# Kernel tuning notes

Measured on AMD Instinct MI355X. Metric: run time of the kernel, lower is better.

The kernel has to match this reference:

```python
import jax, jax.numpy as jnp
import numpy as np

EPS = 1e-5
N_NODES = 50000


def sage_conv(x, src, dst, Wl, Wr, b):
    # mean-aggregate source features at destination nodes, then two linears
    msgs = x[src]  # [E, F] irregular gather
    agg = jax.ops.segment_sum(msgs, dst, num_segments=N_NODES)
    cnt = jax.ops.segment_sum(jnp.ones((src.shape[0], 1), x.dtype), dst,
                              num_segments=N_NODES)
    agg = agg / jnp.maximum(cnt, 1.0)
    return agg @ Wl + x @ Wr + b


def batch_norm(h, gamma, beta):
    mu = jnp.mean(h, axis=0)
    var = jnp.mean((h - mu) ** 2, axis=0)  # biased var, as torch BN training
    return (h - mu) * jax.lax.rsqrt(var + EPS) * gamma + beta


def setup_inputs() -> dict:
    key = jax.random.key(0)
    ks = jax.random.split(key, 16)
    d_in, d_h, n_cls, n_edges = 128, 128, 2, 600000
    s = lambda fan: 1.0 / np.sqrt(fan)
    inp = {
        "x": jax.random.normal(ks[0], (N_NODES, d_in), jnp.float32),
        "edge_index": jax.random.randint(ks[1], (2, n_edges), 0, N_NODES, jnp.int64),
        "W_l0": jax.random.uniform(ks[2], (d_in, d_h), jnp.float32, -s(d_in), s(d_in)),
        "W_r0": jax.random.uniform(ks[3], (d_in, d_h), jnp.float32, -s(d_in), s(d_in)),
        "b0": jnp.zeros((d_h,), jnp.float32),
        "g0": jnp.ones((d_h,), jnp.float32),
        "be0": jnp.zeros((d_h,), jnp.float32),
        "W_l1": jax.random.uniform(ks[4], (d_h, d_h), jnp.float32, -s(d_h), s(d_h)),
        "W_r1": jax.random.uniform(ks[5], (d_h, d_h), jnp.float32, -s(d_h), s(d_h)),
        "b1": jnp.zeros((d_h,), jnp.float32),
        "g1": jnp.ones((d_h,), jnp.float32),
        "be1": jnp.zeros((d_h,), jnp.float32),
        "W_out": jax.random.uniform(ks[6], (d_h, n_cls), jnp.float32, -s(d_h), s(d_h)),
        "b_out": jnp.zeros((n_cls,), jnp.float32),
    }
    return inp


def reference(x, edge_index, W_l0, W_r0, b0, g0, be0,
              W_l1, W_r1, b1, g1, be1, W_out, b_out):
    src, dst = edge_index[0], edge_index[1]
    # layer 0: SAGEConv -> BN -> ReLU (dropout = identity in eval/reference)
    h = sage_conv(x, src, dst, W_l0, W_r0, b0)
    h = jax.nn.relu(batch_norm(h, g0, be0))
    # layer 1
    h = sage_conv(h, src, dst, W_l1, W_r1, b1)
    h = jax.nn.relu(batch_norm(h, g1, be1))
    return h @ W_out + b_out
```

## Files before the change

### kernel.cpp

```cpp
#include <hip/hip_runtime.h>
#include <hip/hip_bf16.h>

#define F 128

typedef __attribute__((ext_vector_type(8))) short short8;
typedef __attribute__((ext_vector_type(4))) float floatx4;

__device__ __forceinline__ float bf_lo(unsigned u) { return __uint_as_float(u << 16); }
__device__ __forceinline__ float bf_hi(unsigned u) { return __uint_as_float(u & 0xffff0000u); }

__device__ __forceinline__ unsigned short f2bf(float x) {
  unsigned u = __float_as_uint(x);
  u += 0x7fffu + ((u >> 16) & 1u);
  return (unsigned short)(u >> 16);
}
__device__ __forceinline__ unsigned pack2(float a, float b) {
  return (unsigned)f2bf(a) | ((unsigned)f2bf(b) << 16);
}

__global__ __launch_bounds__(256) void k_count(const int* __restrict__ dst,
                                               int* __restrict__ A, int E) {
  int e = blockIdx.x * 256 + threadIdx.x;
  if (e < E) atomicAdd(&A[dst[e]], 1);
}

__global__ __launch_bounds__(1024) void k_scanA(int* __restrict__ A,
                                                int* __restrict__ bsum, int n) {
  __shared__ int wtot[16];
  int t = threadIdx.x, l = t & 63, w = t >> 6;
  int i = blockIdx.x * 1024 + t;
  int v = (i < n) ? A[i] : 0;
  int acc = v;
#pragma unroll
  for (int off = 1; off < 64; off <<= 1) {
    int u = __shfl_up(acc, off);
    if (l >= off) acc += u;
  }
  if (l == 63) wtot[w] = acc;
  __syncthreads();
  int woff = 0, total = 0;
#pragma unroll
  for (int ww = 0; ww < 16; ++ww) {
    total += wtot[ww];
    if (ww < w) woff += wtot[ww];
  }
  if (i < n) A[i] = woff + (acc - v);
  if (t == 0) bsum[blockIdx.x] = total;
}

__global__ __launch_bounds__(1024) void k_scanC(int* __restrict__ A,
                                                const int* __restrict__ bsum, int n, int nb) {
  __shared__ int sbase;
  int t = threadIdx.x;
  if (t < 64) {
    int v = (t < nb) ? bsum[t] : 0;
    int acc = v;
#pragma unroll
    for (int off = 1; off < 64; off <<= 1) {
      int u = __shfl_up(acc, off);
      if (t >= off) acc += u;
    }
    int base = (blockIdx.x == 0) ? 0 : __shfl(acc, blockIdx.x - 1);
    if (t == 0) sbase = base;
  }
  __syncthreads();
  int i = blockIdx.x * 1024 + t;
  if (i < n) A[i] += sbase;
}

__global__ __launch_bounds__(256) void k_fill(const int* __restrict__ srcT,
                                              const int* __restrict__ dst,
                                              int* __restrict__ A, int* __restrict__ adj, int E) {
  int e = blockIdx.x * 256 + threadIdx.x;
  if (e >= E) return;
  int s = srcT[e], d = dst[e];
  int slot = atomicAdd(&A[d], 1);
  adj[slot] = s;
}

__global__ __launch_bounds__(256) void k_prep(const float* __restrict__ x,
                                              const float* __restrict__ Wl0,
                                              const float* __restrict__ Wr0,
                                              const float* __restrict__ Wl1,
                                              const float* __restrict__ Wr1,
                                              unsigned short* __restrict__ xb,
                                              unsigned short* __restrict__ WcatT0,
                                              unsigned short* __restrict__ WcatT1, int n4) {
  int i = blockIdx.x * 256 + threadIdx.x;
  if (i < n4) {
    float4 v = ((const float4*)x)[i];
    ((ushort4*)xb)[i] = make_ushort4(f2bf(v.x), f2bf(v.y), f2bf(v.z), f2bf(v.w));
  } else {
    int j = i - n4;
    if (j < 2 * 256 * F) {
      int layer = j >> 15;
      int jj = j & 32767;
      int k = jj >> 7, n = jj & (F - 1);
      const float* Wl = layer ? Wl1 : Wl0;
      const float* Wr = layer ? Wr1 : Wr0;
      unsigned short* WT = layer ? WcatT1 : WcatT0;
      float v = (k < F) ? Wl[k * F + n] : Wr[(k - F) * F + n];
      WT[(size_t)n * 256 + k] = f2bf(v);
    }
  }
}

__global__ __launch_bounds__(256) void k_gather(const unsigned short* __restrict__ xin,
                                                const int* __restrict__ A,
                                                const int* __restrict__ adj,
                                                unsigned short* __restrict__ aggb, int N) {
  int d = blockIdx.x * 4 + (threadIdx.x >> 6);
  if (d >= N) return;
  int l = threadIdx.x & 63;
  int grp = l >> 4, ln = l & 15;
  int e0 = (d == 0) ? 0 : A[d - 1];
  int e1 = A[d];
  int deg = e1 - e0;
  const uint4* xrows = (const uint4*)xin;
  float acc[8] = {0.f, 0.f, 0.f, 0.f, 0.f, 0.f, 0.f, 0.f};
  if (deg > 0) {
    int ids = adj[min(e0 + l, e1 - 1)];
    int m = min(deg, 64);
    for (int j0 = 0; j0 < m; j0 += 4) {
      int jj = j0 + grp;
      int s = __shfl(ids, jj);
      if (jj < m) {
        uint4 u = xrows[(size_t)s * 16 + ln];
        acc[0] += bf_lo(u.x); acc[1] += bf_hi(u.x);
        acc[2] += bf_lo(u.y); acc[3] += bf_hi(u.y);
        acc[4] += bf_lo(u.z); acc[5] += bf_hi(u.z);
        acc[6] += bf_lo(u.w); acc[7] += bf_hi(u.w);
      }
    }
    for (int e = e0 + 64 + grp; e < e1; e += 4) {
      int s = adj[e];
      uint4 u = xrows[(size_t)s * 16 + ln];
      acc[0] += bf_lo(u.x); acc[1] += bf_hi(u.x);
      acc[2] += bf_lo(u.y); acc[3] += bf_hi(u.y);
      acc[4] += bf_lo(u.z); acc[5] += bf_hi(u.z);
      acc[6] += bf_lo(u.w); acc[7] += bf_hi(u.w);
    }
  }
#pragma unroll
  for (int k2 = 0; k2 < 8; ++k2) {
    acc[k2] += __shfl_xor(acc[k2], 16);
    acc[k2] += __shfl_xor(acc[k2], 32);
  }
  if (grp == 0) {
    float inv = 1.0f / fmaxf((float)deg, 1.0f);
    uint4 o = make_uint4(pack2(acc[0] * inv, acc[1] * inv), pack2(acc[2] * inv, acc[3] * inv),
                         pack2(acc[4] * inv, acc[5] * inv), pack2(acc[6] * inv, acc[7] * inv));
    ((uint4*)aggb)[(size_t)d * 16 + ln] = o;
  }
}

__global__ __launch_bounds__(256, 2) void k_gemm(
    const unsigned short* __restrict__ aggb, const unsigned short* __restrict__ xb,
    const unsigned short* __restrict__ WcatT, const float* __restrict__ bias,
    unsigned short* __restrict__ hb, float* __restrict__ pbuf, int N) {
  const int w = threadIdx.x >> 6;
  const int l = threadIdx.x & 63;
  const int lm = l & 15;
  const int lq = l >> 4;
  const int cbase = 32 * w;

  short8 bfrag[2][8];
#pragma unroll
  for (int c = 0; c < 2; ++c) {
    int col = cbase + 16 * c + lm;
    const unsigned short* wp = WcatT + (size_t)col * 256 + lq * 8;
#pragma unroll
    for (int s = 0; s < 8; ++s) bfrag[c][s] = *(const short8*)(wp + 32 * s);
  }
  float bcol0 = bias[cbase + lm];
  float bcol1 = bias[cbase + 16 + lm];
  float bsum0 = 0.f, bsum1 = 0.f, bsq0 = 0.f, bsq1 = 0.f;

  int r0 = blockIdx.x * 64;
  floatx4 acc[4][2] = {};
#pragma unroll
  for (int t = 0; t < 4; ++t) {
    int r = r0 + 16 * t + lm;
    const unsigned short* arow = aggb + (size_t)r * F + lq * 8;
    const unsigned short* xrow = xb + (size_t)r * F + lq * 8;
    short8 af[8];
#pragma unroll
    for (int s = 0; s < 4; ++s) {
      af[s] = *(const short8*)(arow + 32 * s);
      af[s + 4] = *(const short8*)(xrow + 32 * s);
    }
#pragma unroll
    for (int s = 0; s < 8; ++s) {
      acc[t][0] = __builtin_amdgcn_mfma_f32_16x16x32_bf16(af[s], bfrag[0][s], acc[t][0], 0, 0, 0);
      acc[t][1] = __builtin_amdgcn_mfma_f32_16x16x32_bf16(af[s], bfrag[1][s], acc[t][1], 0, 0, 0);
    }
  }
#pragma unroll
  for (int t = 0; t < 4; ++t) {
#pragma unroll
    for (int c = 0; c < 2; ++c) {
      int col = cbase + 16 * c + lm;
      float bc = c ? bcol1 : bcol0;
#pragma unroll
      for (int g = 0; g < 4; ++g) {
        int row = r0 + 16 * t + lq * 4 + g;
        if (row < N) {
          float v = acc[t][c][g] + bc;
          hb[(size_t)row * F + col] = f2bf(v);
          if (c) { bsum1 += v; bsq1 += v * v; }
          else   { bsum0 += v; bsq0 += v * v; }
        }
      }
    }
  }
  bsum0 += __shfl_xor(bsum0, 16); bsum0 += __shfl_xor(bsum0, 32);
  bsq0  += __shfl_xor(bsq0, 16);  bsq0  += __shfl_xor(bsq0, 32);
  bsum1 += __shfl_xor(bsum1, 16); bsum1 += __shfl_xor(bsum1, 32);
  bsq1  += __shfl_xor(bsq1, 16);  bsq1  += __shfl_xor(bsq1, 32);
  if (lq == 0) {
    float* pb = pbuf + (size_t)blockIdx.x * 256;
    pb[cbase + lm]            = bsum0;
    pb[128 + cbase + lm]      = bsq0;
    pb[cbase + 16 + lm]       = bsum1;
    pb[128 + cbase + 16 + lm] = bsq1;
  }
}

__global__ __launch_bounds__(256) void k_bnstats(const float* __restrict__ pbuf,
                                                 const float* __restrict__ g,
                                                 const float* __restrict__ be,
                                                 float* __restrict__ stats,
                                                 float* __restrict__ scale,
                                                 float* __restrict__ shift,
                                                 float invN, int nb) {
  int t = threadIdx.x;
  float s = 0.f;
  for (int b = blockIdx.x; b < nb; b += 8) s += pbuf[(size_t)b * 256 + t];
  atomicAdd(&stats[t], s);
  __threadfence();
  __syncthreads();
  __shared__ int lastS;
  if (t == 0) {
    int ticket = atomicAdd((int*)(stats + 256), 1);
    lastS = (ticket == 7);
  }
  __syncthreads();
  if (lastS) {
    __threadfence();
    if (t < 128) {
      float sum = __hip_atomic_load(&stats[t], __ATOMIC_RELAXED, __HIP_MEMORY_SCOPE_AGENT);
      float sq  = __hip_atomic_load(&stats[t + 128], __ATOMIC_RELAXED, __HIP_MEMORY_SCOPE_AGENT);
      float mu = sum * invN;
      float var = fmaxf(sq * invN - mu * mu, 0.0f);
      float sc = g[t] * rsqrtf(var + 1e-5f);
      scale[t] = sc;
      shift[t] = be[t] - mu * sc;
    }
  }
}

__global__ __launch_bounds__(256) void k_bnrelu(const unsigned short* __restrict__ h,
                                                unsigned short* __restrict__ dst,
                                                const float* __restrict__ scale,
                                                const float* __restrict__ shift, int n8) {
  int i = blockIdx.x * 256 + threadIdx.x;
  if (i >= n8) return;
  uint4 u = ((const uint4*)h)[i];
  int g = i & 15;
  float4 sc0 = ((const float4*)scale)[2 * g];
  float4 sc1 = ((const float4*)scale)[2 * g + 1];
  float4 sh0 = ((const float4*)shift)[2 * g];
  float4 sh1 = ((const float4*)shift)[2 * g + 1];
  unsigned o0 = pack2(fmaxf(fmaf(bf_lo(u.x), sc0.x, sh0.x), 0.f),
                      fmaxf(fmaf(bf_hi(u.x), sc0.y, sh0.y), 0.f));
  unsigned o1 = pack2(fmaxf(fmaf(bf_lo(u.y), sc0.z, sh0.z), 0.f),
                      fmaxf(fmaf(bf_hi(u.y), sc0.w, sh0.w), 0.f));
  unsigned o2 = pack2(fmaxf(fmaf(bf_lo(u.z), sc1.x, sh1.x), 0.f),
                      fmaxf(fmaf(bf_hi(u.z), sc1.y, sh1.y), 0.f));
  unsigned o3 = pack2(fmaxf(fmaf(bf_lo(u.w), sc1.z, sh1.z), 0.f),
                      fmaxf(fmaf(bf_hi(u.w), sc1.w, sh1.w), 0.f));
  ((uint4*)dst)[i] = make_uint4(o0, o1, o2, o3);
}

__global__ __launch_bounds__(256) void k_bnout(const unsigned short* __restrict__ hb,
                                               const float* __restrict__ scale,
                                               const float* __restrict__ shift,
                                               const float* __restrict__ Wout,
                                               const float* __restrict__ bout,
                                               float* __restrict__ out, int N) {
  __shared__ float W0s[F], W1s[F];
  int t = threadIdx.x;
  if (t < F) {
    W0s[t] = Wout[2 * t];
    W1s[t] = Wout[2 * t + 1];
  }
  __syncthreads();
  int r = blockIdx.x * 16 + (t >> 4);
  int ln = t & 15;
  if (r >= N) return;
  uint4 u = ((const uint4*)(hb + (size_t)r * F))[ln];
  float4 sc0 = ((const float4*)scale)[2 * ln];
  float4 sc1 = ((const float4*)scale)[2 * ln + 1];
  float4 sh0 = ((const float4*)shift)[2 * ln];
  float4 sh1 = ((const float4*)shift)[2 * ln + 1];
  float v[8];
  v[0] = fmaxf(fmaf(bf_lo(u.x), sc0.x, sh0.x), 0.f);
  v[1] = fmaxf(fmaf(bf_hi(u.x), sc0.y, sh0.y), 0.f);
  v[2] = fmaxf(fmaf(bf_lo(u.y), sc0.z, sh0.z), 0.f);
  v[3] = fmaxf(fmaf(bf_hi(u.y), sc0.w, sh0.w), 0.f);
  v[4] = fmaxf(fmaf(bf_lo(u.z), sc1.x, sh1.x), 0.f);
  v[5] = fmaxf(fmaf(bf_hi(u.z), sc1.y, sh1.y), 0.f);
  v[6] = fmaxf(fmaf(bf_lo(u.w), sc1.z, sh1.z), 0.f);
  v[7] = fmaxf(fmaf(bf_hi(u.w), sc1.w, sh1.w), 0.f);
  float a0 = 0.f, a1 = 0.f;
#pragma unroll
  for (int j = 0; j < 8; ++j) {
    a0 += v[j] * W0s[8 * ln + j];
    a1 += v[j] * W1s[8 * ln + j];
  }
#pragma unroll
  for (int off = 1; off < 16; off <<= 1) {
    a0 += __shfl_xor(a0, off);
    a1 += __shfl_xor(a1, off);
  }
  if (ln == 0) {
    out[2 * r]     = a0 + bout[0];
    out[2 * r + 1] = a1 + bout[1];
  }
}

extern "C" void kernel_launch(void* const* d_in, const int* in_sizes, int n_in,
                              void* d_out, int out_size, void* d_ws, size_t ws_size,
                              hipStream_t stream) {
  const float* x   = (const float*)d_in[0];
  const int*   eix = (const int*)d_in[1];
  const float* Wl0 = (const float*)d_in[2];
  const float* Wr0 = (const float*)d_in[3];
  const float* b0  = (const float*)d_in[4];
  const float* g0  = (const float*)d_in[5];
  const float* be0 = (const float*)d_in[6];
  const float* Wl1 = (const float*)d_in[7];
  const float* Wr1 = (const float*)d_in[8];
  const float* b1  = (const float*)d_in[9];
  const float* g1  = (const float*)d_in[10];
  const float* be1 = (const float*)d_in[11];
  const float* Wo  = (const float*)d_in[12];
  const float* bo  = (const float*)d_in[13];

  int N = in_sizes[0] / F;
  int E = in_sizes[1] / 2;
  const int* src  = eix;
  const int* dstv = eix + E;

  int nRowBlocks = (N + 63) / 64;
  size_t Npad = (size_t)nRowBlocks * 64;
  int nScanB = (N + 1023) / 1024;

  unsigned short* aggb   = (unsigned short*)d_ws;
  unsigned short* xb     = aggb + Npad * F;
  unsigned short* hb     = xb + Npad * F;
  unsigned short* WcatT0 = hb + Npad * F;
  unsigned short* WcatT1 = WcatT0 + 256 * F;
  float* scale  = (float*)(WcatT1 + 256 * F);
  float* shift  = scale + F;
  int*   A      = (int*)(shift + F);
  int*   bsum   = A + N;
  float* stats0 = (float*)(bsum + 64);
  float* stats1 = stats0 + 257;
  int*   adj    = (int*)(stats1 + 257);
  float* pbuf   = (float*)(adj + E);

  hipMemsetAsync(A, 0, (size_t)(N + 64 + 514) * sizeof(int), stream);

  k_count<<<(E + 255) / 256, 256, 0, stream>>>(dstv, A, E);
  k_scanA<<<nScanB, 1024, 0, stream>>>(A, bsum, N);
  k_scanC<<<nScanB, 1024, 0, stream>>>(A, bsum, N, nScanB);
  k_fill<<<(E + 255) / 256, 256, 0, stream>>>(src, dstv, A, adj, E);

  int n4 = N * F / 4, n8 = N * F / 8;
  k_prep<<<(n4 + 2 * 256 * F + 255) / 256, 256, 0, stream>>>(x, Wl0, Wr0, Wl1, Wr1,
                                                             xb, WcatT0, WcatT1, n4);

  k_gather<<<(N + 3) / 4, 256, 0, stream>>>(xb, A, adj, aggb, N);
  k_gemm<<<nRowBlocks, 256, 0, stream>>>(aggb, xb, WcatT0, b0, hb, pbuf, N);
  k_bnstats<<<8, 256, 0, stream>>>(pbuf, g0, be0, stats0, scale, shift, 1.0f / N, nRowBlocks);
  k_bnrelu<<<(n8 + 255) / 256, 256, 0, stream>>>(hb, xb, scale, shift, n8);

  k_gather<<<(N + 3) / 4, 256, 0, stream>>>(xb, A, adj, aggb, N);
  k_gemm<<<nRowBlocks, 256, 0, stream>>>(aggb, xb, WcatT1, b1, hb, pbuf, N);
  k_bnstats<<<8, 256, 0, stream>>>(pbuf, g1, be1, stats1, scale, shift, 1.0f / N, nRowBlocks);

  k_bnout<<<(N + 15) / 16, 256, 0, stream>>>(hb, scale, shift, Wo, bo, (float*)d_out, N);
}
```

Baseline: 343.2 us.

## Fuse neighbor gather, GEMM and BN stats into one per-layer kernel

Each layer's mean-aggregation gather now writes its bf16 result into LDS, and the same block runs the MFMA GEMM from there. The separate global agg buffer and its write/read round-trip go away. BN statistics reduction moves into the layer kernel's tail via a last-block ticket, and the degree-count kernel is merged into the prep conversion kernel, cutting launches. The risk is that the gather phase, now inside a 2-occupancy GEMM kernel holding register-resident weight fragments, may get less latency hiding. The last block also serially sums all per-block partials.

```diff
diff --git a/kernel.cpp b/kernel.cpp
--- a/kernel.cpp
+++ b/kernel.cpp
@@ -18,75 +18,22 @@
   return (unsigned)f2bf(a) | ((unsigned)f2bf(b) << 16);
 }
 
-__global__ __launch_bounds__(256) void k_count(const int* __restrict__ dst,
-                                               int* __restrict__ A, int E) {
-  int e = blockIdx.x * 256 + threadIdx.x;
-  if (e < E) atomicAdd(&A[dst[e]], 1);
-}
-
-__global__ __launch_bounds__(1024) void k_scanA(int* __restrict__ A,
-                                                int* __restrict__ bsum, int n) {
-  __shared__ int wtot[16];
-  int t = threadIdx.x, l = t & 63, w = t >> 6;
-  int i = blockIdx.x * 1024 + t;
-  int v = (i < n) ? A[i] : 0;
-  int acc = v;
-#pragma unroll
-  for (int off = 1; off < 64; off <<= 1) {
-    int u = __shfl_up(acc, off);
-    if (l >= off) acc += u;
-  }
-  if (l == 63) wtot[w] = acc;
-  __syncthreads();
-  int woff = 0, total = 0;
-#pragma unroll
-  for (int ww = 0; ww < 16; ++ww) {
-    total += wtot[ww];
-    if (ww < w) woff += wtot[ww];
-  }
-  if (i < n) A[i] = woff + (acc - v);
-  if (t == 0) bsum[blockIdx.x] = total;
-}
-
-__global__ __launch_bounds__(1024) void k_scanC(int* __restrict__ A,
-                                                const int* __restrict__ bsum, int n, int nb) {
-  __shared__ int sbase;
-  int t = threadIdx.x;
-  if (t < 64) {
-    int v = (t < nb) ? bsum[t] : 0;
-    int acc = v;
-#pragma unroll
-    for (int off = 1; off < 64; off <<= 1) {
-      int u = __shfl_up(acc, off);
-      if (t >= off) acc += u;
-    }
-    int base = (blockIdx.x == 0) ? 0 : __shfl(acc, blockIdx.x - 1);
-    if (t == 0) sbase = base;
-  }
-  __syncthreads();
-  int i = blockIdx.x * 1024 + t;
-  if (i < n) A[i] += sbase;
-}
-
-__global__ __launch_bounds__(256) void k_fill(const int* __restrict__ srcT,
-                                              const int* __restrict__ dst,
-                                              int* __restrict__ A, int* __restrict__ adj, int E) {
-  int e = blockIdx.x * 256 + threadIdx.x;
-  if (e >= E) return;
-  int s = srcT[e], d = dst[e];
-  int slot = atomicAdd(&A[d], 1);
-  adj[slot] = s;
-}
-
-__global__ __launch_bounds__(256) void k_prep(const float* __restrict__ x,
-                                              const float* __restrict__ Wl0,
-                                              const float* __restrict__ Wr0,
-                                              const float* __restrict__ Wl1,
-                                              const float* __restrict__ Wr1,
-                                              unsigned short* __restrict__ xb,
-                                              unsigned short* __restrict__ WcatT0,
-                                              unsigned short* __restrict__ WcatT1, int n4) {
-  int i = blockIdx.x * 256 + threadIdx.x;
+__global__ __launch_bounds__(256) void k_pre(const int* __restrict__ dst, int* __restrict__ A,
+                                             int E, int cb,
+                                             const float* __restrict__ x,
+                                             const float* __restrict__ Wl0,
+                                             const float* __restrict__ Wr0,
+                                             const float* __restrict__ Wl1,
+                                             const float* __restrict__ Wr1,
+                                             unsigned short* __restrict__ xb,
+                                             unsigned short* __restrict__ WcatT0,
+                                             unsigned short* __restrict__ WcatT1, int n4) {
+  if (blockIdx.x < cb) {
+    int e = blockIdx.x * 256 + threadIdx.x;
+    if (e < E) atomicAdd(&A[dst[e]], 1);
+    return;
+  }
+  int i = (blockIdx.x - cb) * 256 + threadIdx.x;
   if (i < n4) {
     float4 v = ((const float4*)x)[i];
     ((ushort4*)xb)[i] = make_ushort4(f2bf(v.x), f2bf(v.y), f2bf(v.z), f2bf(v.w));
@@ -105,84 +52,143 @@
   }
 }
 
-__global__ __launch_bounds__(256) void k_gather(const unsigned short* __restrict__ xin,
-                                                const int* __restrict__ A,
-                                                const int* __restrict__ adj,
-                                                unsigned short* __restrict__ aggb, int N) {
-  int d = blockIdx.x * 4 + (threadIdx.x >> 6);
-  if (d >= N) return;
-  int l = threadIdx.x & 63;
-  int grp = l >> 4, ln = l & 15;
-  int e0 = (d == 0) ? 0 : A[d - 1];
-  int e1 = A[d];
-  int deg = e1 - e0;
-  const uint4* xrows = (const uint4*)xin;
-  float acc[8] = {0.f, 0.f, 0.f, 0.f, 0.f, 0.f, 0.f, 0.f};
-  if (deg > 0) {
-    int ids = adj[min(e0 + l, e1 - 1)];
-    int m = min(deg, 64);
-    for (int j0 = 0; j0 < m; j0 += 4) {
-      int jj = j0 + grp;
-      int s = __shfl(ids, jj);
-      if (jj < m) {
-        uint4 u = xrows[(size_t)s * 16 + ln];
-        acc[0] += bf_lo(u.x); acc[1] += bf_hi(u.x);
-        acc[2] += bf_lo(u.y); acc[3] += bf_hi(u.y);
-        acc[4] += bf_lo(u.z); acc[5] += bf_hi(u.z);
-        acc[6] += bf_lo(u.w); acc[7] += bf_hi(u.w);
+__global__ __launch_bounds__(1024) void k_scanA(int* __restrict__ A,
+                                                int* __restrict__ bsum, int n) {
+  __shared__ int wtot[16];
+  int t = threadIdx.x, l = t & 63, w = t >> 6;
+  int i = blockIdx.x * 1024 + t;
+  int v = (i < n) ? A[i] : 0;
+  int acc = v;
+#pragma unroll
+  for (int off = 1; off < 64; off <<= 1) {
+    int u = __shfl_up(acc, off);
+    if (l >= off) acc += u;
+  }
+  if (l == 63) wtot[w] = acc;
+  __syncthreads();
+  int woff = 0, total = 0;
+#pragma unroll
+  for (int ww = 0; ww < 16; ++ww) {
+    total += wtot[ww];
+    if (ww < w) woff += wtot[ww];
+  }
+  if (i < n) A[i] = woff + (acc - v);
+  if (t == 0) bsum[blockIdx.x] = total;
+}
+
+__global__ __launch_bounds__(1024) void k_scanC(int* __restrict__ A,
+                                                const int* __restrict__ bsum, int n, int nb) {
+  __shared__ int sbase;
+  int t = threadIdx.x;
+  if (t < 64) {
+    int v = (t < nb) ? bsum[t] : 0;
+    int acc = v;
+#pragma unroll
+    for (int off = 1; off < 64; off <<= 1) {
+      int u = __shfl_up(acc, off);
+      if (t >= off) acc += u;
+    }
+    int base = (blockIdx.x == 0) ? 0 : __shfl(acc, blockIdx.x - 1);
+    if (t == 0) sbase = base;
+  }
+  __syncthreads();
+  int i = blockIdx.x * 1024 + t;
+  if (i < n) A[i] += sbase;
+}
+
+__global__ __launch_bounds__(256) void k_fill(const int* __restrict__ srcT,
+                                              const int* __restrict__ dst,
+                                              int* __restrict__ A, int* __restrict__ adj, int E) {
+  int e = blockIdx.x * 256 + threadIdx.x;
+  if (e >= E) return;
+  int s = srcT[e], d = dst[e];
+  int slot = atomicAdd(&A[d], 1);
+  adj[slot] = s;
+}
+
+__global__ __launch_bounds__(256, 2) void k_layer(
+    const unsigned short* __restrict__ xin, const int* __restrict__ A,
+    const int* __restrict__ adj, const unsigned short* __restrict__ WcatT,
+    const float* __restrict__ bias, unsigned short* __restrict__ hb,
+    float* __restrict__ pbuf, int* __restrict__ ticket,
+    const float* __restrict__ g, const float* __restrict__ be,
+    float* __restrict__ scale, float* __restrict__ shift,
+    float invN, int N, int nb) {
+  __shared__ unsigned short aggS[64][136];
+  __shared__ float red[256];
+  __shared__ int lastS;
+  const int tid = threadIdx.x;
+  const int w = tid >> 6, l = tid & 63;
+  const int grp = l >> 4, ln = l & 15;
+  const int cbase = 32 * w;
+  const int r0 = blockIdx.x * 64;
+
+  short8 bfrag[2][8];
+#pragma unroll
+  for (int c = 0; c < 2; ++c) {
+    int col = cbase + 16 * c + ln;
+    const unsigned short* wp = WcatT + (size_t)col * 256 + grp * 8;
+#pragma unroll
+    for (int s = 0; s < 8; ++s) bfrag[c][s] = *(const short8*)(wp + 32 * s);
+  }
+  float bcol0 = bias[cbase + ln];
+  float bcol1 = bias[cbase + 16 + ln];
+
+  const uint4* xrows4 = (const uint4*)xin;
+#pragma unroll 1
+  for (int i = 0; i < 16; ++i) {
+    int dd = w + 4 * i;
+    int d = r0 + dd;
+    float acc[8] = {0.f, 0.f, 0.f, 0.f, 0.f, 0.f, 0.f, 0.f};
+    int deg = 0;
+    if (d < N) {
+      int e0 = (d == 0) ? 0 : A[d - 1];
+      int e1 = A[d];
+      deg = e1 - e0;
+      if (deg > 0) {
+        int ids = adj[min(e0 + l, e1 - 1)];
+        int m = min(deg, 64);
+        for (int j0 = 0; j0 < m; j0 += 4) {
+          int jj = j0 + grp;
+          int s = __shfl(ids, jj);
+          if (jj < m) {
+            uint4 u = xrows4[(size_t)s * 16 + ln];
+            acc[0] += bf_lo(u.x); acc[1] += bf_hi(u.x);
+            acc[2] += bf_lo(u.y); acc[3] += bf_hi(u.y);
+            acc[4] += bf_lo(u.z); acc[5] += bf_hi(u.z);
+            acc[6] += bf_lo(u.w); acc[7] += bf_hi(u.w);
+          }
+        }
+        for (int e = e0 + 64 + grp; e < e1; e += 4) {
+          int s = adj[e];
+          uint4 u = xrows4[(size_t)s * 16 + ln];
+          acc[0] += bf_lo(u.x); acc[1] += bf_hi(u.x);
+          acc[2] += bf_lo(u.y); acc[3] += bf_hi(u.y);
+          acc[4] += bf_lo(u.z); acc[5] += bf_hi(u.z);
+          acc[6] += bf_lo(u.w); acc[7] += bf_hi(u.w);
+        }
       }
     }
-    for (int e = e0 + 64 + grp; e < e1; e += 4) {
-      int s = adj[e];
-      uint4 u = xrows[(size_t)s * 16 + ln];
-      acc[0] += bf_lo(u.x); acc[1] += bf_hi(u.x);
-      acc[2] += bf_lo(u.y); acc[3] += bf_hi(u.y);
-      acc[4] += bf_lo(u.z); acc[5] += bf_hi(u.z);
-      acc[6] += bf_lo(u.w); acc[7] += bf_hi(u.w);
-    }
-  }
-#pragma unroll
-  for (int k2 = 0; k2 < 8; ++k2) {
-    acc[k2] += __shfl_xor(acc[k2], 16);
-    acc[k2] += __shfl_xor(acc[k2], 32);
-  }
-  if (grp == 0) {
-    float inv = 1.0f / fmaxf((float)deg, 1.0f);
-    uint4 o = make_uint4(pack2(acc[0] * inv, acc[1] * inv), pack2(acc[2] * inv, acc[3] * inv),
-                         pack2(acc[4] * inv, acc[5] * inv), pack2(acc[6] * inv, acc[7] * inv));
-    ((uint4*)aggb)[(size_t)d * 16 + ln] = o;
-  }
-}
-
-__global__ __launch_bounds__(256, 2) void k_gemm(
-    const unsigned short* __restrict__ aggb, const unsigned short* __restrict__ xb,
-    const unsigned short* __restrict__ WcatT, const float* __restrict__ bias,
-    unsigned short* __restrict__ hb, float* __restrict__ pbuf, int N) {
-  const int w = threadIdx.x >> 6;
-  const int l = threadIdx.x & 63;
-  const int lm = l & 15;
-  const int lq = l >> 4;
-  const int cbase = 32 * w;
-
-  short8 bfrag[2][8];
-#pragma unroll
-  for (int c = 0; c < 2; ++c) {
-    int col = cbase + 16 * c + lm;
-    const unsigned short* wp = WcatT + (size_t)col * 256 + lq * 8;
-#pragma unroll
-    for (int s = 0; s < 8; ++s) bfrag[c][s] = *(const short8*)(wp + 32 * s);
-  }
-  float bcol0 = bias[cbase + lm];
-  float bcol1 = bias[cbase + 16 + lm];
+#pragma unroll
+    for (int k2 = 0; k2 < 8; ++k2) {
+      acc[k2] += __shfl_xor(acc[k2], 16);
+      acc[k2] += __shfl_xor(acc[k2], 32);
+    }
+    if (grp == 0) {
+      float inv = 1.0f / fmaxf((float)deg, 1.0f);
+      uint4 o = make_uint4(pack2(acc[0] * inv, acc[1] * inv), pack2(acc[2] * inv, acc[3] * inv),
+                           pack2(acc[4] * inv, acc[5] * inv), pack2(acc[6] * inv, acc[7] * inv));
+      *(uint4*)(&aggS[dd][ln * 8]) = o;
+    }
+  }
+  __syncthreads();
+
   float bsum0 = 0.f, bsum1 = 0.f, bsq0 = 0.f, bsq1 = 0.f;
-
-  int r0 = blockIdx.x * 64;
-  floatx4 acc[4][2] = {};
+  floatx4 acc2[4][2] = {};
 #pragma unroll
   for (int t = 0; t < 4; ++t) {
-    int r = r0 + 16 * t + lm;
-    const unsigned short* arow = aggb + (size_t)r * F + lq * 8;
-    const unsigned short* xrow = xb + (size_t)r * F + lq * 8;
+    const unsigned short* arow = &aggS[16 * t + ln][grp * 8];
+    const unsigned short* xrow = xin + (size_t)(r0 + 16 * t + ln) * F + grp * 8;
     short8 af[8];
 #pragma unroll
     for (int s = 0; s < 4; ++s) {
@@ -191,21 +197,21 @@
     }
 #pragma unroll
     for (int s = 0; s < 8; ++s) {
-      acc[t][0] = __builtin_amdgcn_mfma_f32_16x16x32_bf16(af[s], bfrag[0][s], acc[t][0], 0, 0, 0);
-      acc[t][1] = __builtin_amdgcn_mfma_f32_16x16x32_bf16(af[s], bfrag[1][s], acc[t][1], 0, 0, 0);
+      acc2[t][0] = __builtin_amdgcn_mfma_f32_16x16x32_bf16(af[s], bfrag[0][s], acc2[t][0], 0, 0, 0);
+      acc2[t][1] = __builtin_amdgcn_mfma_f32_16x16x32_bf16(af[s], bfrag[1][s], acc2[t][1], 0, 0, 0);
     }
   }
 #pragma unroll
   for (int t = 0; t < 4; ++t) {
 #pragma unroll
     for (int c = 0; c < 2; ++c) {
-      int col = cbase + 16 * c + lm;
+      int col = cbase + 16 * c + ln;
       float bc = c ? bcol1 : bcol0;
 #pragma unroll
-      for (int g = 0; g < 4; ++g) {
-        int row = r0 + 16 * t + lq * 4 + g;
+      for (int gg = 0; gg < 4; ++gg) {
+        int row = r0 + 16 * t + grp * 4 + gg;
         if (row < N) {
-          float v = acc[t][c][g] + bc;
+          float v = acc2[t][c][gg] + bc;
           hb[(size_t)row * F + col] = f2bf(v);
           if (c) { bsum1 += v; bsq1 += v * v; }
           else   { bsum0 += v; bsq0 += v * v; }
@@ -217,44 +223,33 @@
   bsq0  += __shfl_xor(bsq0, 16);  bsq0  += __shfl_xor(bsq0, 32);
   bsum1 += __shfl_xor(bsum1, 16); bsum1 += __shfl_xor(bsum1, 32);
   bsq1  += __shfl_xor(bsq1, 16);  bsq1  += __shfl_xor(bsq1, 32);
-  if (lq == 0) {
+  if (grp == 0) {
     float* pb = pbuf + (size_t)blockIdx.x * 256;
-    pb[cbase + lm]            = bsum0;
-    pb[128 + cbase + lm]      = bsq0;
-    pb[cbase + 16 + lm]       = bsum1;
-    pb[128 + cbase + 16 + lm] = bsq1;
-  }
-}
-
-__global__ __launch_bounds__(256) void k_bnstats(const float* __restrict__ pbuf,
-                                                 const float* __restrict__ g,
-                                                 const float* __restrict__ be,
-                                                 float* __restrict__ stats,
-                                                 float* __restrict__ scale,
-                                                 float* __restrict__ shift,
-                                                 float invN, int nb) {
-  int t = threadIdx.x;
-  float s = 0.f;
-  for (int b = blockIdx.x; b < nb; b += 8) s += pbuf[(size_t)b * 256 + t];
-  atomicAdd(&stats[t], s);
+    __hip_atomic_store(&pb[cbase + ln], bsum0, __ATOMIC_RELAXED, __HIP_MEMORY_SCOPE_AGENT);
+    __hip_atomic_store(&pb[128 + cbase + ln], bsq0, __ATOMIC_RELAXED, __HIP_MEMORY_SCOPE_AGENT);
+    __hip_atomic_store(&pb[cbase + 16 + ln], bsum1, __ATOMIC_RELAXED, __HIP_MEMORY_SCOPE_AGENT);
+    __hip_atomic_store(&pb[128 + cbase + 16 + ln], bsq1, __ATOMIC_RELAXED, __HIP_MEMORY_SCOPE_AGENT);
+  }
   __threadfence();
   __syncthreads();
-  __shared__ int lastS;
-  if (t == 0) {
-    int ticket = atomicAdd((int*)(stats + 256), 1);
-    lastS = (ticket == 7);
+  if (tid == 0) {
+    int tk = __hip_atomic_fetch_add(ticket, 1, __ATOMIC_ACQ_REL, __HIP_MEMORY_SCOPE_AGENT);
+    lastS = (tk == nb - 1);
   }
   __syncthreads();
   if (lastS) {
     __threadfence();
-    if (t < 128) {
-      float sum = __hip_atomic_load(&stats[t], __ATOMIC_RELAXED, __HIP_MEMORY_SCOPE_AGENT);
-      float sq  = __hip_atomic_load(&stats[t + 128], __ATOMIC_RELAXED, __HIP_MEMORY_SCOPE_AGENT);
-      float mu = sum * invN;
-      float var = fmaxf(sq * invN - mu * mu, 0.0f);
-      float sc = g[t] * rsqrtf(var + 1e-5f);
-      scale[t] = sc;
-      shift[t] = be[t] - mu * sc;
+    float s = 0.f;
+    for (int b = 0; b < nb; ++b)
+      s += __hip_atomic_load(&pbuf[(size_t)b * 256 + tid], __ATOMIC_RELAXED, __HIP_MEMORY_SCOPE_AGENT);
+    red[tid] = s;
+    __syncthreads();
+    if (tid < 128) {
+      float mu = red[tid] * invN;
+      float var = fmaxf(red[tid + 128] * invN - mu * mu, 0.0f);
+      float sc = g[tid] * rsqrtf(var + 1e-5f);
+      scale[tid] = sc;
+      shift[tid] = be[tid] - mu * sc;
     }
   }
 }
@@ -356,8 +351,7 @@
   size_t Npad = (size_t)nRowBlocks * 64;
   int nScanB = (N + 1023) / 1024;
 
-  unsigned short* aggb   = (unsigned short*)d_ws;
-  unsigned short* xb     = aggb + Npad * F;
+  unsigned short* xb     = (unsigned short*)d_ws;
   unsigned short* hb     = xb + Npad * F;
   unsigned short* WcatT0 = hb + Npad * F;
   unsigned short* WcatT1 = WcatT0 + 256 * F;
@@ -372,23 +366,24 @@
 
   hipMemsetAsync(A, 0, (size_t)(N + 64 + 514) * sizeof(int), stream);
 
-  k_count<<<(E + 255) / 256, 256, 0, stream>>>(dstv, A, E);
+  int n4 = N * F / 4, n8 = N * F / 8;
+  int cb = (E + 255) / 256;
+
+  k_pre<<<cb + (n4 + 2 * 256 * F + 255) / 256, 256, 0, stream>>>(
+      dstv, A, E, cb, x, Wl0, Wr0, Wl1, Wr1, xb, WcatT0, WcatT1, n4);
+
   k_scanA<<<nScanB, 1024, 0, stream>>>(A, bsum, N);
   k_scanC<<<nScanB, 1024, 0, stream>>>(A, bsum, N, nScanB);
   k_fill<<<(E + 255) / 256, 256, 0, stream>>>(src, dstv, A, adj, E);
 
-  int n4 = N * F / 4, n8 = N * F / 8;
-  k_prep<<<(n4 + 2 * 256 * F + 255) / 256, 256, 0, stream>>>(x, Wl0, Wr0, Wl1, Wr1,
-                                                             xb, WcatT0, WcatT1, n4);
-
-  k_gather<<<(N + 3) / 4, 256, 0, stream>>>(xb, A, adj, aggb, N);
-  k_gemm<<<nRowBlocks, 256, 0, stream>>>(aggb, xb, WcatT0, b0, hb, pbuf, N);
-  k_bnstats<<<8, 256, 0, stream>>>(pbuf, g0, be0, stats0, scale, shift, 1.0f / N, nRowBlocks);
+  k_layer<<<nRowBlocks, 256, 0, stream>>>(xb, A, adj, WcatT0, b0, hb, pbuf,
+                                          (int*)(stats0 + 256), g0, be0, scale, shift,
+                                          1.0f / N, N, nRowBlocks);
   k_bnrelu<<<(n8 + 255) / 256, 256, 0, stream>>>(hb, xb, scale, shift, n8);
 
-  k_gather<<<(N + 3) / 4, 256, 0, stream>>>(xb, A, adj, aggb, N);
-  k_gemm<<<nRowBlocks, 256, 0, stream>>>(aggb, xb, WcatT1, b1, hb, pbuf, N);
-  k_bnstats<<<8, 256, 0, stream>>>(pbuf, g1, be1, stats1, scale, shift, 1.0f / N, nRowBlocks);
+  k_layer<<<nRowBlocks, 256, 0, stream>>>(xb, A, adj, WcatT1, b1, hb, pbuf,
+                                          (int*)(stats1 + 256), g1, be1, scale, shift,
+                                          1.0f / N, N, nRowBlocks);
 
   k_bnout<<<(N + 15) / 16, 256, 0, stream>>>(hb, scale, shift, Wo, bo, (float*)d_out, N);
 }
```

New measurement: 905.6 us. +163.9%, slower.
